# Kernel tuning notes

Hardware: AMD Instinct MI355X
Metric: run time of the kernel (lower is better)

## Reference

```python
import jax, jax.numpy as jnp
import numpy as np

B, C, H, W = 4, 512, 64, 64
CQ = C // 8


def setup_inputs() -> dict:
    key = jax.random.key(0)
    ks = jax.random.split(key, 8)
    s_in = 1.0 / np.sqrt(C)
    return {
        "x": jax.random.normal(ks[0], (B, C, H, W), jnp.float32),
        "wq": jax.random.normal(ks[1], (CQ, C), jnp.float32) * s_in,
        "bq": jax.random.normal(ks[2], (CQ,), jnp.float32) * 0.01,
        "wk": jax.random.normal(ks[3], (CQ, C), jnp.float32) * s_in,
        "bk": jax.random.normal(ks[4], (CQ,), jnp.float32) * 0.01,
        "wv": jax.random.normal(ks[5], (C, C), jnp.float32) * s_in,
        "bv": jax.random.normal(ks[6], (C,), jnp.float32) * 0.01,
        "gamma": jax.random.normal(ks[7], (1,), jnp.float32) * 0.1,
    }


def reference(x, wq, bq, wk, bk, wv, bv, gamma):
    b, c, h, w = x.shape
    n = h * w
    xf = x.reshape(b, c, n)  # [B, C, N]; 1x1 conv == channel matmul
    q = jnp.einsum("oc,bcn->bon", wq, xf) + bq[None, :, None]  # [B, CQ, N]
    k = jnp.einsum("oc,bcn->bon", wk, xf) + bk[None, :, None]  # [B, CQ, N]
    v = jnp.einsum("oc,bcn->bon", wv, xf) + bv[None, :, None]  # [B, C, N]
    energy = jnp.einsum("bcn,bcm->bnm", q, k)  # [B, N, N]
    attn = jax.nn.softmax(energy, axis=-1)
    out = jnp.einsum("bcm,bnm->bcn", v, attn)  # [B, C, N]
    out = out.reshape(b, c, h, w)
    return gamma[0] * out + x
```

## Files before the change

### kernel.cpp

```cpp
#include <hip/hip_runtime.h>
#include <hip/hip_bf16.h>

#define BATCH 4
#define CH    512
#define NPIX  4096
#define LOG2E 1.4426950408889634f

#define BOFF  327680
#define WTOT  328320
#define PSTR  268

typedef float v4f __attribute__((ext_vector_type(4)));
typedef short v8s __attribute__((ext_vector_type(8)));
typedef unsigned short u16;

__device__ __forceinline__ float b2f(u16 v){
    union { unsigned u; float f; } x; x.u = ((unsigned)v) << 16; return x.f;
}
__device__ __forceinline__ u16 f2b(float f){
    union { float f; unsigned u; } x; x.f = f;
    unsigned r = x.u + 0x7fffu + ((x.u >> 16) & 1u);
    return (u16)(r >> 16);
}
__device__ __forceinline__ void f2b2(float a, float b, u16* o){
    union { __hip_bfloat162 v; u16 s[2]; } u;
    u.v = __float22bfloat162_rn(make_float2(a, b));
    o[0] = u.s[0]; o[1] = u.s[1];
}
__device__ __forceinline__ float fexp2(float x){
#if __has_builtin(__builtin_amdgcn_exp2f)
    return __builtin_amdgcn_exp2f(x);
#else
    return exp2f(x);
#endif
}
__device__ __forceinline__ v4f mfma16(v8s a, v8s b, v4f c){
    return __builtin_amdgcn_mfma_f32_16x16x32_bf16(a, b, c, 0, 0, 0);
}
__device__ __forceinline__ float load_s(const void* p, size_t idx, int isf32){
    return isf32 ? ((const float*)p)[idx] : b2f(((const u16*)p)[idx]);
}

__global__ void detect_kernel(const unsigned* __restrict__ x, int* __restrict__ flag){
    __shared__ int cnt;
    if (threadIdx.x == 0) cnt = 0;
    __syncthreads();
    int c = 0;
    for (int i = threadIdx.x; i < 1024; i += 64){
        unsigned e = (x[i] >> 23) & 0xFFu;
        if (e >= 64u && e < 192u) c++;
    }
    atomicAdd(&cnt, c);
    __syncthreads();
    if (threadIdx.x == 0) flag[0] = (cnt > 512) ? 1 : 0;
}

__global__ __launch_bounds__(256) void prep_kernel(
    const void* __restrict__ wq, const void* __restrict__ bq,
    const void* __restrict__ wk, const void* __restrict__ bk,
    const void* __restrict__ wv, const void* __restrict__ bv,
    u16* __restrict__ wall, const int* __restrict__ flag)
{
    const int isf32 = flag[0];
    int i = blockIdx.x * 256 + threadIdx.x;
    if (i >= WTOT) return;
    float v;
    if (i < BOFF){
        int o = i >> 9, c = i & 511;
        if (o < 64)       v = load_s(wq, (size_t)o * 512 + c, isf32);
        else if (o < 128) v = load_s(wk, (size_t)(o - 64) * 512 + c, isf32);
        else              v = load_s(wv, (size_t)(o - 128) * 512 + c, isf32);
    } else {
        int o = i - BOFF;
        if (o < 64)       v = load_s(bq, o, isf32);
        else if (o < 128) v = load_s(bk, o - 64, isf32);
        else              v = load_s(bv, o - 128, isf32);
    }
    wall[i] = f2b(v);
}

__global__ __launch_bounds__(256, 2) void proj_kernel(
    const void* __restrict__ x, const u16* __restrict__ wall,
    u16* __restrict__ Qf, u16* __restrict__ Kf, u16* __restrict__ Vf,
    u16* __restrict__ xbf, const int* __restrict__ flag)
{
    const int isf32 = flag[0];
    const int ntile = blockIdx.x, os = blockIdx.y, b = blockIdx.z;
    const int n0 = ntile * 64;
    const int t = threadIdx.x, lane = t & 63, w = t >> 6, q = lane >> 4, col = lane & 15;

    __shared__ __align__(16) u16 xT[2][64 * 40];

    const int rrow  = t >> 3;
    const int ncol8 = (t & 7) * 8;
    const int xswz  = (t & 3) << 3;
    const size_t xbase = (size_t)b * CH * NPIX + n0 + ncol8;

    v4f acc[5][4];
    #pragma unroll
    for (int i = 0; i < 5; i++)
        #pragma unroll
        for (int j = 0; j < 4; j++) acc[i][j] = (v4f){0.f, 0.f, 0.f, 0.f};

    float4 gn0, gn1;

    #define LOADX(cb_) do {                                                  \
        const size_t src = xbase + (size_t)((cb_) * 32 + rrow) * NPIX;       \
        if (isf32){ gn0 = *(const float4*)((const float*)x + src);           \
                    gn1 = *(const float4*)((const float*)x + src + 4); }     \
        else { union { uint4 v; float4 f; } lu;                              \
               lu.v = *(const uint4*)((const u16*)x + src); gn0 = lu.f; }    \
    } while (0)

    #define CVT8(vals_) do {                                                 \
        if (isf32){ f2b2(gn0.x, gn0.y, &vals_[0]); f2b2(gn0.z, gn0.w, &vals_[2]); \
                    f2b2(gn1.x, gn1.y, &vals_[4]); f2b2(gn1.z, gn1.w, &vals_[6]); } \
        else { union { float4 f; uint4 v; } uu; uu.f = gn0;                  \
               *(uint4*)vals_ = uu.v; }                                      \
    } while (0)

    {
        LOADX(0);
        u16 vals[8]; CVT8(vals);
        #pragma unroll
        for (int i = 0; i < 8; i++) xT[0][(ncol8 + i) * 40 + (rrow ^ xswz)] = vals[i];
        if (os == 0)
            *(uint4*)&xbf[(size_t)(b * CH + rrow) * NPIX + n0 + ncol8] = *(uint4*)vals;
        LOADX(1);
    }
    __syncthreads();

    for (int cb = 0; cb < 16; cb++){
        const int buf = cb & 1;
        const int c0 = cb * 32 + q * 8;

        v8s wf[5];
        #pragma unroll
        for (int ct = 0; ct < 5; ct++)
            wf[ct] = *(const v8s*)&wall[(size_t)(320 * os + 80 * w + 16 * ct + col) * 512 + c0];

        v8s a[4];
        #pragma unroll
        for (int g = 0; g < 4; g++){
            const int rsw = ((2 * g + (col >> 3)) & 3) << 3;
            a[g] = *(const v8s*)&xT[buf][(16 * g + col) * 40 + (rsw ^ (q * 8))];
        }

        if (cb < 15){
            u16 vals[8]; CVT8(vals);
            #pragma unroll
            for (int i = 0; i < 8; i++) xT[buf ^ 1][(ncol8 + i) * 40 + (rrow ^ xswz)] = vals[i];
            if (os == 0)
                *(uint4*)&xbf[(size_t)(b * CH + (cb + 1) * 32 + rrow) * NPIX + n0 + ncol8] = *(uint4*)vals;
            if (cb < 14) LOADX(cb + 2);
        }

        #pragma unroll
        for (int ct = 0; ct < 5; ct++)
            #pragma unroll
            for (int g = 0; g < 4; g++)
                acc[ct][g] = mfma16(a[g], wf[ct], acc[ct][g]);
        __syncthreads();
    }
    #undef LOADX
    #undef CVT8

    const u16* ball = wall + BOFF;
    #pragma unroll
    for (int ct = 0; ct < 5; ct++){
        const int o = 320 * os + 80 * w + 16 * ct + col;
        const float bv_ = b2f(ball[o]);
        #pragma unroll
        for (int g = 0; g < 4; g++){
            const int nb = n0 + 16 * g + 4 * q;
            if (o < 64){
                const int k = o;
                size_t base = (size_t)b * NPIX * 64
                    + ((size_t)((nb >> 4) * 2 + (k >> 5))) * 512
                    + ((k & 31) >> 3) * 128 + (nb & 15) * 8 + (k & 7);
                #pragma unroll
                for (int r = 0; r < 4; r++)
                    Qf[base + r * 8] = f2b((acc[ct][g][r] + bv_) * LOG2E);
            } else if (o < 128){
                const int k = o - 64;
                size_t base = (size_t)b * NPIX * 64
                    + ((size_t)((nb >> 4) * 2 + (k >> 5))) * 512
                    + ((k & 31) >> 3) * 128 + (nb & 15) * 8 + (k & 7);
                #pragma unroll
                for (int r = 0; r < 4; r++)
                    Kf[base + r * 8] = f2b(acc[ct][g][r] + bv_);
            } else {
                const int c = o - 128;
                size_t base = (size_t)b * CH * NPIX
                    + ((size_t)((c >> 4) * 128 + (nb >> 5))) * 512
                    + ((nb & 31) >> 3) * 128 + (c & 15) * 8 + (nb & 7);
                union { uint2 u; u16 s[4]; } ov;
                #pragma unroll
                for (int r = 0; r < 4; r++)
                    ov.s[r] = f2b(acc[ct][g][r] + bv_);
                *(uint2*)&Vf[base] = ov.u;
            }
        }
    }
}

__global__ __launch_bounds__(512, 4) void attn_kernel(
    const u16* __restrict__ Qf, const u16* __restrict__ Kf, const u16* __restrict__ Vf,
    const u16* __restrict__ xbf, const void* __restrict__ gamma,
    void* __restrict__ out, const int* __restrict__ flag)
{
    const int isf32 = flag[0];
    const int bid = blockIdx.x;
    const int csplit = bid & 1;
    const int b      = (bid >> 1) & 3;
    const int ntile  = bid >> 3;
    const int n0 = ntile * 64;

    const int t = threadIdx.x, lane = t & 63, w = t >> 6, q = lane >> 4, col = lane & 15;

    __shared__ __align__(16) u16  Plds[2][64 * PSTR];
    __shared__ __align__(16) float lsum[8][64];

    const u16* Qb = Qf + (size_t)b * NPIX * 64;
    const u16* Kb = Kf + (size_t)b * NPIX * 64;
    const u16* Vb = Vf + (size_t)b * CH * NPIX;

    v8s qa[4][2];
    #pragma unroll
    for (int g = 0; g < 4; g++)
        #pragma unroll
        for (int c2 = 0; c2 < 2; c2++)
            qa[g][c2] = *(const v8s*)&Qb[(size_t)(((n0 >> 4) + g) * 2 + c2) * 512 + lane * 8];

    float lreg[4] = {0.f, 0.f, 0.f, 0.f};

    v4f oacc[2][4];
    #pragma unroll
    for (int i = 0; i < 2; i++)
        #pragma unroll
        for (int j = 0; j < 4; j++) oacc[i][j] = (v4f){0.f, 0.f, 0.f, 0.f};

    const int ms    = 32 * w;
    const int cslab = csplit * 256 + 32 * w;

    for (int it = 0; it < 16; it++){
        const int m0 = it * 256;
        const int buf = it & 1;

        v8s va_c[2];
        #pragma unroll
        for (int ct = 0; ct < 2; ct++)
            va_c[ct] = *(const v8s*)&Vb[(size_t)(((cslab + 16 * ct) >> 4) * 128 + (m0 >> 5)) * 512 + lane * 8];

        v8s kf[2][2];
        #pragma unroll
        for (int mt = 0; mt < 2; mt++)
            #pragma unroll
            for (int c2 = 0; c2 < 2; c2++)
                kf[mt][c2] = *(const v8s*)&Kb[(size_t)((((m0 + ms) >> 4) + mt) * 2 + c2) * 512 + lane * 8];

        #pragma unroll
        for (int g = 0; g < 4; g++){
            #pragma unroll
            for (int mt = 0; mt < 2; mt++){
                v4f sv = (v4f){-64.f, -64.f, -64.f, -64.f};
                sv = mfma16(kf[mt][0], qa[g][0], sv);
                sv = mfma16(kf[mt][1], qa[g][1], sv);
                float p0 = fexp2(sv[0]), p1 = fexp2(sv[1]);
                float p2 = fexp2(sv[2]), p3 = fexp2(sv[3]);
                lreg[g] += (p0 + p1) + (p2 + p3);
                union { uint2 u; u16 s[4]; } pk;
                f2b2(p0, p1, &pk.s[0]);
                f2b2(p2, p3, &pk.s[2]);
                *(uint2*)&Plds[buf][(16 * g + col) * PSTR + ms + 16 * mt + 4 * q] = pk.u;
            }
        }

        __syncthreads();

        #pragma unroll
        for (int kk = 0; kk < 8; kk++){
            v8s va_n[2];
            if (kk < 7){
                #pragma unroll
                for (int ct = 0; ct < 2; ct++)
                    va_n[ct] = *(const v8s*)&Vb[(size_t)(((cslab + 16 * ct) >> 4) * 128 + (m0 >> 5) + kk + 1) * 512 + lane * 8];
            }
            v8s pb[4];
            #pragma unroll
            for (int nt = 0; nt < 4; nt++)
                pb[nt] = *(const v8s*)&Plds[buf][(16 * nt + col) * PSTR + 32 * kk + q * 8];
            __builtin_amdgcn_s_setprio(1);
            #pragma unroll
            for (int ct = 0; ct < 2; ct++)
                #pragma unroll
                for (int nt = 0; nt < 4; nt++)
                    oacc[ct][nt] = mfma16(va_c[ct], pb[nt], oacc[ct][nt]);
            __builtin_amdgcn_s_setprio(0);
            #pragma unroll
            for (int ct = 0; ct < 2; ct++) va_c[ct] = va_n[ct];
        }
    }

    #pragma unroll
    for (int g = 0; g < 4; g++){
        lreg[g] += __shfl_xor(lreg[g], 16);
        lreg[g] += __shfl_xor(lreg[g], 32);
    }
    if (lane < 16){
        #pragma unroll
        for (int g = 0; g < 4; g++)
            lsum[w][16 * g + lane] = lreg[g];
    }
    __syncthreads();

    const float gam = load_s(gamma, 0, isf32);
    float linv[4];
    #pragma unroll
    for (int nt = 0; nt < 4; nt++){
        int nn = 16 * nt + col;
        float l = ((lsum[0][nn] + lsum[1][nn]) + (lsum[2][nn] + lsum[3][nn]))
                + ((lsum[4][nn] + lsum[5][nn]) + (lsum[6][nn] + lsum[7][nn]));
        linv[nt] = gam / l;
    }

    const size_t boff = (size_t)b * CH * NPIX;
    #pragma unroll
    for (int ct = 0; ct < 2; ct++){
        #pragma unroll
        for (int rr = 0; rr < 4; rr++){
            int c = cslab + 16 * ct + 4 * q + rr;
            size_t base = boff + (size_t)c * NPIX + n0;
            #pragma unroll
            for (int nt = 0; nt < 4; nt++){
                int n = 16 * nt + col;
                float o = oacc[ct][nt][rr] * linv[nt] + b2f(xbf[base + n]);
                if (isf32) ((float*)out)[base + n] = o;
                else       ((u16*)out)[base + n]  = f2b(o);
            }
        }
    }
}

extern "C" void kernel_launch(void* const* d_in, const int* in_sizes, int n_in,
                              void* d_out, int out_size, void* d_ws, size_t ws_size,
                              hipStream_t stream)
{
    const void* x     = d_in[0];
    const void* wq    = d_in[1];
    const void* bq    = d_in[2];
    const void* wk    = d_in[3];
    const void* bk    = d_in[4];
    const void* wv    = d_in[5];
    const void* bv    = d_in[6];
    const void* gamma = d_in[7];

    u16* Qf   = (u16*)d_ws;
    u16* Kf   = Qf + (size_t)1048576;
    u16* Vf   = Kf + (size_t)1048576;
    u16* xbf  = Vf + (size_t)8388608;
    u16* wall = xbf + (size_t)8388608;
    int* flag = (int*)(wall + WTOT + 16);

    detect_kernel<<<1, 64, 0, stream>>>((const unsigned*)x, flag);
    prep_kernel<<<(WTOT + 255) / 256, 256, 0, stream>>>(wq, bq, wk, bk, wv, bv, wall, flag);
    proj_kernel<<<dim3(64, 2, BATCH), 256, 0, stream>>>(x, wall, Qf, Kf, Vf, xbf, flag);
    attn_kernel<<<512, 512, 0, stream>>>(Qf, Kf, Vf, xbf, gamma, d_out, flag);
}
```

Before: 208.5 us.

## Software-pipeline QK/exp with PV MFMAs and fold dtype detection into kernels

The attention main loop is restructured so the energy MFMAs and exp for the next 256-key tile are computed while the PV MFMAs consume the current P tile. A prologue and epilogue handle the first and last tiles, and there is now one barrier per iteration. Separately, the standalone detect kernel launch is removed: every block re-sniffs the input dtype from the first 1024 words of x with a wave reduction. This saves one launch but adds redundant global reads and a barrier in every block.

```diff
diff --git a/kernel.cpp b/kernel.cpp
--- a/kernel.cpp
+++ b/kernel.cpp
@@ -41,27 +41,31 @@
     return isf32 ? ((const float*)p)[idx] : b2f(((const u16*)p)[idx]);
 }
 
-__global__ void detect_kernel(const unsigned* __restrict__ x, int* __restrict__ flag){
-    __shared__ int cnt;
-    if (threadIdx.x == 0) cnt = 0;
+__device__ __forceinline__ int sniff_isf32(const unsigned* __restrict__ xw,
+                                           int t, int nthr, int* cnt){
+    if (t == 0) *cnt = 0;
     __syncthreads();
     int c = 0;
-    for (int i = threadIdx.x; i < 1024; i += 64){
-        unsigned e = (x[i] >> 23) & 0xFFu;
+    for (int i = t; i < 1024; i += nthr){
+        unsigned e = (xw[i] >> 23) & 0xFFu;
         if (e >= 64u && e < 192u) c++;
     }
-    atomicAdd(&cnt, c);
+    c += __shfl_xor(c, 1);  c += __shfl_xor(c, 2);  c += __shfl_xor(c, 4);
+    c += __shfl_xor(c, 8);  c += __shfl_xor(c, 16); c += __shfl_xor(c, 32);
+    if ((t & 63) == 0) atomicAdd(cnt, c);
     __syncthreads();
-    if (threadIdx.x == 0) flag[0] = (cnt > 512) ? 1 : 0;
+    return (*cnt > 512) ? 1 : 0;
 }
 
 __global__ __launch_bounds__(256) void prep_kernel(
     const void* __restrict__ wq, const void* __restrict__ bq,
     const void* __restrict__ wk, const void* __restrict__ bk,
     const void* __restrict__ wv, const void* __restrict__ bv,
-    u16* __restrict__ wall, const int* __restrict__ flag)
+    const void* __restrict__ x, u16* __restrict__ wall)
 {
-    const int isf32 = flag[0];
+    __shared__ int scnt;
+    const int isf32 = sniff_isf32((const unsigned*)x, threadIdx.x, 256, &scnt);
+
     int i = blockIdx.x * 256 + threadIdx.x;
     if (i >= WTOT) return;
     float v;
@@ -82,14 +86,16 @@
 __global__ __launch_bounds__(256, 2) void proj_kernel(
     const void* __restrict__ x, const u16* __restrict__ wall,
     u16* __restrict__ Qf, u16* __restrict__ Kf, u16* __restrict__ Vf,
-    u16* __restrict__ xbf, const int* __restrict__ flag)
+    u16* __restrict__ xbf)
 {
-    const int isf32 = flag[0];
+    __shared__ __align__(16) u16 xT[2][64 * 40];
+    __shared__ int scnt;
+
+    const int isf32 = sniff_isf32((const unsigned*)x, threadIdx.x, 256, &scnt);
+
     const int ntile = blockIdx.x, os = blockIdx.y, b = blockIdx.z;
     const int n0 = ntile * 64;
     const int t = threadIdx.x, lane = t & 63, w = t >> 6, q = lane >> 4, col = lane & 15;
-
-    __shared__ __align__(16) u16 xT[2][64 * 40];
 
     const int rrow  = t >> 3;
     const int ncol8 = (t & 7) * 8;
@@ -205,11 +211,17 @@
 }
 
 __global__ __launch_bounds__(512, 4) void attn_kernel(
+    const void* __restrict__ x,
     const u16* __restrict__ Qf, const u16* __restrict__ Kf, const u16* __restrict__ Vf,
     const u16* __restrict__ xbf, const void* __restrict__ gamma,
-    void* __restrict__ out, const int* __restrict__ flag)
+    void* __restrict__ out)
 {
-    const int isf32 = flag[0];
+    __shared__ __align__(16) u16  Plds[2][64 * PSTR];
+    __shared__ __align__(16) float lsum[8][64];
+    __shared__ int scnt;
+
+    const int isf32 = sniff_isf32((const unsigned*)x, threadIdx.x, 512, &scnt);
+
     const int bid = blockIdx.x;
     const int csplit = bid & 1;
     const int b      = (bid >> 1) & 3;
@@ -218,9 +230,6 @@
 
     const int t = threadIdx.x, lane = t & 63, w = t >> 6, q = lane >> 4, col = lane & 15;
 
-    __shared__ __align__(16) u16  Plds[2][64 * PSTR];
-    __shared__ __align__(16) float lsum[8][64];
-
     const u16* Qb = Qf + (size_t)b * NPIX * 64;
     const u16* Kb = Kf + (size_t)b * NPIX * 64;
     const u16* Vb = Vf + (size_t)b * CH * NPIX;
@@ -243,26 +252,71 @@
     const int ms    = 32 * w;
     const int cslab = csplit * 256 + 32 * w;
 
-    for (int it = 0; it < 16; it++){
+    {
+        v8s kf0[2][2];
+        #pragma unroll
+        for (int mt = 0; mt < 2; mt++)
+            #pragma unroll
+            for (int c2 = 0; c2 < 2; c2++)
+                kf0[mt][c2] = *(const v8s*)&Kb[(size_t)(((ms >> 4) + mt) * 2 + c2) * 512 + lane * 8];
+        #pragma unroll
+        for (int g = 0; g < 4; g++){
+            #pragma unroll
+            for (int mt = 0; mt < 2; mt++){
+                v4f sv = (v4f){-64.f, -64.f, -64.f, -64.f};
+                sv = mfma16(kf0[mt][0], qa[g][0], sv);
+                sv = mfma16(kf0[mt][1], qa[g][1], sv);
+                float p0 = fexp2(sv[0]), p1 = fexp2(sv[1]);
+                float p2 = fexp2(sv[2]), p3 = fexp2(sv[3]);
+                lreg[g] += (p0 + p1) + (p2 + p3);
+                union { uint2 u; u16 s[4]; } pk;
+                f2b2(p0, p1, &pk.s[0]);
+                f2b2(p2, p3, &pk.s[2]);
+                *(uint2*)&Plds[0][(16 * g + col) * PSTR + ms + 16 * mt + 4 * q] = pk.u;
+            }
+        }
+    }
+
+    for (int it = 0; it < 15; it++){
+        __syncthreads();
+        const int buf = it & 1;
         const int m0 = it * 256;
-        const int buf = it & 1;
+        const int m1 = m0 + 256;
+
+        v8s kf[2][2];
+        #pragma unroll
+        for (int mt = 0; mt < 2; mt++)
+            #pragma unroll
+            for (int c2 = 0; c2 < 2; c2++)
+                kf[mt][c2] = *(const v8s*)&Kb[(size_t)((((m1 + ms) >> 4) + mt) * 2 + c2) * 512 + lane * 8];
 
         v8s va_c[2];
         #pragma unroll
         for (int ct = 0; ct < 2; ct++)
             va_c[ct] = *(const v8s*)&Vb[(size_t)(((cslab + 16 * ct) >> 4) * 128 + (m0 >> 5)) * 512 + lane * 8];
 
-        v8s kf[2][2];
-        #pragma unroll
-        for (int mt = 0; mt < 2; mt++)
-            #pragma unroll
-            for (int c2 = 0; c2 < 2; c2++)
-                kf[mt][c2] = *(const v8s*)&Kb[(size_t)((((m0 + ms) >> 4) + mt) * 2 + c2) * 512 + lane * 8];
-
-        #pragma unroll
-        for (int g = 0; g < 4; g++){
-            #pragma unroll
-            for (int mt = 0; mt < 2; mt++){
+        #pragma unroll
+        for (int kk = 0; kk < 8; kk++){
+            v8s va_n[2];
+            if (kk < 7){
+                #pragma unroll
+                for (int ct = 0; ct < 2; ct++)
+                    va_n[ct] = *(const v8s*)&Vb[(size_t)(((cslab + 16 * ct) >> 4) * 128 + (m0 >> 5) + kk + 1) * 512 + lane * 8];
+            }
+            v8s pb[4];
+            #pragma unroll
+            for (int nt = 0; nt < 4; nt++)
+                pb[nt] = *(const v8s*)&Plds[buf][(16 * nt + col) * PSTR + 32 * kk + q * 8];
+            __builtin_amdgcn_s_setprio(1);
+            #pragma unroll
+            for (int ct = 0; ct < 2; ct++)
+                #pragma unroll
+                for (int nt = 0; nt < 4; nt++)
+                    oacc[ct][nt] = mfma16(va_c[ct], pb[nt], oacc[ct][nt]);
+            __builtin_amdgcn_s_setprio(0);
+
+            {
+                const int g = kk >> 1, mt = kk & 1;
                 v4f sv = (v4f){-64.f, -64.f, -64.f, -64.f};
                 sv = mfma16(kf[mt][0], qa[g][0], sv);
                 sv = mfma16(kf[mt][1], qa[g][1], sv);
@@ -272,12 +326,21 @@
                 union { uint2 u; u16 s[4]; } pk;
                 f2b2(p0, p1, &pk.s[0]);
                 f2b2(p2, p3, &pk.s[2]);
-                *(uint2*)&Plds[buf][(16 * g + col) * PSTR + ms + 16 * mt + 4 * q] = pk.u;
-            }
-        }
-
+                *(uint2*)&Plds[buf ^ 1][(16 * g + col) * PSTR + ms + 16 * mt + 4 * q] = pk.u;
+            }
+
+            #pragma unroll
+            for (int ct = 0; ct < 2; ct++) va_c[ct] = va_n[ct];
+        }
+    }
+
+    {
         __syncthreads();
-
+        const int m0 = 15 * 256;
+        v8s va_c[2];
+        #pragma unroll
+        for (int ct = 0; ct < 2; ct++)
+            va_c[ct] = *(const v8s*)&Vb[(size_t)(((cslab + 16 * ct) >> 4) * 128 + (m0 >> 5)) * 512 + lane * 8];
         #pragma unroll
         for (int kk = 0; kk < 8; kk++){
             v8s va_n[2];
@@ -289,7 +352,7 @@
             v8s pb[4];
             #pragma unroll
             for (int nt = 0; nt < 4; nt++)
-                pb[nt] = *(const v8s*)&Plds[buf][(16 * nt + col) * PSTR + 32 * kk + q * 8];
+                pb[nt] = *(const v8s*)&Plds[1][(16 * nt + col) * PSTR + 32 * kk + q * 8];
             __builtin_amdgcn_s_setprio(1);
             #pragma unroll
             for (int ct = 0; ct < 2; ct++)
@@ -360,10 +423,8 @@
     u16* Vf   = Kf + (size_t)1048576;
     u16* xbf  = Vf + (size_t)8388608;
     u16* wall = xbf + (size_t)8388608;
-    int* flag = (int*)(wall + WTOT + 16);
-
-    detect_kernel<<<1, 64, 0, stream>>>((const unsigned*)x, flag);
-    prep_kernel<<<(WTOT + 255) / 256, 256, 0, stream>>>(wq, bq, wk, bk, wv, bv, wall, flag);
-    proj_kernel<<<dim3(64, 2, BATCH), 256, 0, stream>>>(x, wall, Qf, Kf, Vf, xbf, flag);
-    attn_kernel<<<512, 512, 0, stream>>>(Qf, Kf, Vf, xbf, gamma, d_out, flag);
-}
+
+    prep_kernel<<<(WTOT + 255) / 256, 256, 0, stream>>>(wq, bq, wk, bk, wv, bv, x, wall);
+    proj_kernel<<<dim3(64, 2, BATCH), 256, 0, stream>>>(x, wall, Qf, Kf, Vf, xbf);
+    attn_kernel<<<512, 512, 0, stream>>>(x, Qf, Kf, Vf, xbf, gamma, d_out);
+}
```

Result: slower. 310.4 us (+48.8%).

## Fold dtype detection into each kernel and drop separate detect launch

Applied to the files above, without the earlier changes.

Removes the single-block detect kernel and instead has every block of prep, proj and attn sniff the input dtype itself from the first 1024 words of x, using a wave shuffle reduction. This eliminates one kernel launch and its serialization in the stream. The cost is redundant reads and a block barrier at the start of every block. It also raises proj occupancy hint to 3 blocks per CU and moves the first V fragment load after the barrier in the attention loop.

```diff
diff --git a/kernel.cpp b/kernel.cpp
--- a/kernel.cpp
+++ b/kernel.cpp
@@ -41,27 +41,31 @@
     return isf32 ? ((const float*)p)[idx] : b2f(((const u16*)p)[idx]);
 }
 
-__global__ void detect_kernel(const unsigned* __restrict__ x, int* __restrict__ flag){
-    __shared__ int cnt;
-    if (threadIdx.x == 0) cnt = 0;
+__device__ __forceinline__ int sniff_isf32(const unsigned* __restrict__ xw,
+                                           int t, int nthr, int* cnt){
+    if (t == 0) *cnt = 0;
     __syncthreads();
     int c = 0;
-    for (int i = threadIdx.x; i < 1024; i += 64){
-        unsigned e = (x[i] >> 23) & 0xFFu;
+    for (int i = t; i < 1024; i += nthr){
+        unsigned e = (xw[i] >> 23) & 0xFFu;
         if (e >= 64u && e < 192u) c++;
     }
-    atomicAdd(&cnt, c);
+    c += __shfl_xor(c, 1);  c += __shfl_xor(c, 2);  c += __shfl_xor(c, 4);
+    c += __shfl_xor(c, 8);  c += __shfl_xor(c, 16); c += __shfl_xor(c, 32);
+    if ((t & 63) == 0) atomicAdd(cnt, c);
     __syncthreads();
-    if (threadIdx.x == 0) flag[0] = (cnt > 512) ? 1 : 0;
+    return (*cnt > 512) ? 1 : 0;
 }
 
 __global__ __launch_bounds__(256) void prep_kernel(
     const void* __restrict__ wq, const void* __restrict__ bq,
     const void* __restrict__ wk, const void* __restrict__ bk,
     const void* __restrict__ wv, const void* __restrict__ bv,
-    u16* __restrict__ wall, const int* __restrict__ flag)
+    const void* __restrict__ x, u16* __restrict__ wall)
 {
-    const int isf32 = flag[0];
+    __shared__ int scnt;
+    const int isf32 = sniff_isf32((const unsigned*)x, threadIdx.x, 256, &scnt);
+
     int i = blockIdx.x * 256 + threadIdx.x;
     if (i >= WTOT) return;
     float v;
@@ -79,17 +83,19 @@
     wall[i] = f2b(v);
 }
 
-__global__ __launch_bounds__(256, 2) void proj_kernel(
+__global__ __launch_bounds__(256, 3) void proj_kernel(
     const void* __restrict__ x, const u16* __restrict__ wall,
     u16* __restrict__ Qf, u16* __restrict__ Kf, u16* __restrict__ Vf,
-    u16* __restrict__ xbf, const int* __restrict__ flag)
+    u16* __restrict__ xbf)
 {
-    const int isf32 = flag[0];
+    __shared__ __align__(16) u16 xT[2][64 * 40];
+    __shared__ int scnt;
+
+    const int isf32 = sniff_isf32((const unsigned*)x, threadIdx.x, 256, &scnt);
+
     const int ntile = blockIdx.x, os = blockIdx.y, b = blockIdx.z;
     const int n0 = ntile * 64;
     const int t = threadIdx.x, lane = t & 63, w = t >> 6, q = lane >> 4, col = lane & 15;
-
-    __shared__ __align__(16) u16 xT[2][64 * 40];
 
     const int rrow  = t >> 3;
     const int ncol8 = (t & 7) * 8;
@@ -205,11 +211,17 @@
 }
 
 __global__ __launch_bounds__(512, 4) void attn_kernel(
+    const void* __restrict__ x,
     const u16* __restrict__ Qf, const u16* __restrict__ Kf, const u16* __restrict__ Vf,
     const u16* __restrict__ xbf, const void* __restrict__ gamma,
-    void* __restrict__ out, const int* __restrict__ flag)
+    void* __restrict__ out)
 {
-    const int isf32 = flag[0];
+    __shared__ __align__(16) u16  Plds[2][64 * PSTR];
+    __shared__ __align__(16) float lsum[8][64];
+    __shared__ int scnt;
+
+    const int isf32 = sniff_isf32((const unsigned*)x, threadIdx.x, 512, &scnt);
+
     const int bid = blockIdx.x;
     const int csplit = bid & 1;
     const int b      = (bid >> 1) & 3;
@@ -218,9 +230,6 @@
 
     const int t = threadIdx.x, lane = t & 63, w = t >> 6, q = lane >> 4, col = lane & 15;
 
-    __shared__ __align__(16) u16  Plds[2][64 * PSTR];
-    __shared__ __align__(16) float lsum[8][64];
-
     const u16* Qb = Qf + (size_t)b * NPIX * 64;
     const u16* Kb = Kf + (size_t)b * NPIX * 64;
     const u16* Vb = Vf + (size_t)b * CH * NPIX;
@@ -246,11 +255,6 @@
     for (int it = 0; it < 16; it++){
         const int m0 = it * 256;
         const int buf = it & 1;
-
-        v8s va_c[2];
-        #pragma unroll
-        for (int ct = 0; ct < 2; ct++)
-            va_c[ct] = *(const v8s*)&Vb[(size_t)(((cslab + 16 * ct) >> 4) * 128 + (m0 >> 5)) * 512 + lane * 8];
 
         v8s kf[2][2];
         #pragma unroll
@@ -278,6 +282,10 @@
 
         __syncthreads();
 
+        v8s va_c[2];
+        #pragma unroll
+        for (int ct = 0; ct < 2; ct++)
+            va_c[ct] = *(const v8s*)&Vb[(size_t)(((cslab + 16 * ct) >> 4) * 128 + (m0 >> 5)) * 512 + lane * 8];
         #pragma unroll
         for (int kk = 0; kk < 8; kk++){
             v8s va_n[2];
@@ -360,10 +368,8 @@
     u16* Vf   = Kf + (size_t)1048576;
     u16* xbf  = Vf + (size_t)8388608;
     u16* wall = xbf + (size_t)8388608;
-    int* flag = (int*)(wall + WTOT + 16);
-
-    detect_kernel<<<1, 64, 0, stream>>>((const unsigned*)x, flag);
-    prep_kernel<<<(WTOT + 255) / 256, 256, 0, stream>>>(wq, bq, wk, bk, wv, bv, wall, flag);
-    proj_kernel<<<dim3(64, 2, BATCH), 256, 0, stream>>>(x, wall, Qf, Kf, Vf, xbf, flag);
-    attn_kernel<<<512, 512, 0, stream>>>(Qf, Kf, Vf, xbf, gamma, d_out, flag);
-}
+
+    prep_kernel<<<(WTOT + 255) / 256, 256, 0, stream>>>(wq, bq, wk, bk, wv, bv, x, wall);
+    proj_kernel<<<dim3(64, 2, BATCH), 256, 0, stream>>>(x, wall, Qf, Kf, Vf, xbf);
+    attn_kernel<<<512, 512, 0, stream>>>(x, Qf, Kf, Vf, xbf, gamma, d_out);
+}
```

Result: no change. 207.6 us (-0.4%).
